# Performance work log

Hardware: AMD Instinct MI355X
Metric: run time of the kernel (lower is better)

The kernel has to match this reference:

```python
import jax, jax.numpy as jnp
import numpy as np

D_EMB = 1024
N_HEAD = 16


def setup_inputs() -> dict:
    key = jax.random.key(0)
    k0, k1, k2, k3, k4, k5 = jax.random.split(key, 6)
    B, T, D = 2, 2048, D_EMB
    s = 1.0 / np.sqrt(D)
    x = jax.random.normal(k0, (B, T, D), dtype=jnp.float32)
    # torch Linear params: weight [out, in], bias [out]
    w_attn = jax.random.normal(k1, (3 * D, D), dtype=jnp.float32) * s
    b_attn = jax.random.normal(k2, (3 * D,), dtype=jnp.float32) * 0.01
    w_proj = jax.random.normal(k3, (D, D), dtype=jnp.float32) * s
    b_proj = jax.random.normal(k4, (D,), dtype=jnp.float32) * 0.01
    return {"x": x, "w_attn": w_attn, "b_attn": b_attn,
            "w_proj": w_proj, "b_proj": b_proj}


def reference(x, w_attn, b_attn, w_proj, b_proj):
    B, T, D = x.shape
    H = N_HEAD
    hd = D // H
    qkv = x @ w_attn.T + b_attn  # [B, T, 3D]
    q, k, v = jnp.split(qkv, 3, axis=-1)
    # 'b t (h d) -> b h t d'
    q = q.reshape(B, T, H, hd).transpose(0, 2, 1, 3)
    k = k.reshape(B, T, H, hd).transpose(0, 2, 1, 3)
    v = v.reshape(B, T, H, hd).transpose(0, 2, 1, 3)
    scale = 1.0 / np.sqrt(hd)
    scores = jnp.einsum('bhid,bhjd->bhij', q, k) * scale  # [B,H,T,T]
    scores = scores.astype(jnp.float32)
    # NOTE: source applies NO causal mask despite the class name
    attn = jax.nn.softmax(scores, axis=-1)
    out = jnp.einsum('bhij,bhjd->bhid', attn, v)  # [B,H,T,hd]
    out = out.transpose(0, 2, 1, 3).reshape(B, T, D)  # 'b h i d -> b i (h d)'
    y = out @ w_proj.T + b_proj
    return y
```

## Files before the change

### kernel.cpp

```cpp
#include <hip/hip_runtime.h>


typedef unsigned short u16;
typedef __bf16  bf16x8 __attribute__((ext_vector_type(8)));
typedef float   f32x4  __attribute__((ext_vector_type(4)));
typedef float   f32x16 __attribute__((ext_vector_type(16)));
typedef unsigned short u16x8 __attribute__((ext_vector_type(8)));
typedef unsigned int   u32x4 __attribute__((ext_vector_type(4)));

__device__ __forceinline__ u16 f2bf(float f) {
  __bf16 h = (__bf16)f;
  return __builtin_bit_cast(unsigned short, h);
}
__device__ __forceinline__ float bf2f(u16 u) {
  unsigned int x = ((unsigned int)u) << 16;
  return __builtin_bit_cast(float, x);
}
__device__ __forceinline__ f32x4 mfma16(u16x8 a, u16x8 b, f32x4 c) {
  return __builtin_amdgcn_mfma_f32_16x16x32_bf16(
      __builtin_bit_cast(bf16x8, a), __builtin_bit_cast(bf16x8, b), c, 0, 0, 0);
}
__device__ __forceinline__ f32x16 mfma32(u16x8 a, u16x8 b, f32x16 c) {
  return __builtin_amdgcn_mfma_f32_32x32x16_bf16(
      __builtin_bit_cast(bf16x8, a), __builtin_bit_cast(bf16x8, b), c, 0, 0, 0);
}
__device__ __forceinline__ void gld_lds16(const void* g, void* l) {
  __builtin_amdgcn_global_load_lds(
      (const __attribute__((address_space(1))) void*)g,
      (__attribute__((address_space(3))) void*)l, 16, 0, 0);
}
__device__ __forceinline__ unsigned pack_bf2(float lo, float hi) {
  unsigned r;
  asm("v_cvt_pk_bf16_f32 %0, %1, %2" : "=v"(r) : "v"(lo), "v"(hi));
  return r;
}
__device__ __forceinline__ void xhalf(unsigned &Wl, unsigned &Wh, bool hib) {
  unsigned sel = hib ? Wl : Wh;
  unsigned p   = (unsigned)__shfl_xor((int)sel, 32);
  unsigned nl  = hib ? p  : Wl;
  unsigned nh  = hib ? Wh : p;
  Wl = nl; Wh = nh;
}

__global__ __launch_bounds__(256) void cvt_f32_bf16(
    const float* __restrict__ in, u16* __restrict__ out, int n4) {
  int i = blockIdx.x * blockDim.x + threadIdx.x;
  if (i < n4) {
    float4 v = ((const float4*)in)[i];
    ushort4 o;
    o.x = f2bf(v.x); o.y = f2bf(v.y); o.z = f2bf(v.z); o.w = f2bf(v.w);
    ((ushort4*)out)[i] = o;
  }
}

__device__ __forceinline__ void gemm_tile(
    const u16* __restrict__ A, const u16* __restrict__ B, const int K,
    const int bm, const int bn, u16* As, u16* Bs, f32x4 acc[4][4]) {
  const int tid  = threadIdx.x;
  const int lane = tid & 63;
  const int wv   = tid >> 6;
  const int wr   = wv >> 1, wc = wv & 1;
  const int g    = lane >> 4, lc = lane & 15;
  const int nk   = K >> 5;
  for (int kt = 0; kt < nk; ++kt) {
    __syncthreads();
#pragma unroll
    for (int it = 0; it < 2; ++it) {
      const int c  = it * 4 + wv;
      const int r  = c * 16 + (lane >> 2);
      const int cc = lane & 3;
      gld_lds16(A + (size_t)(bm + r) * K + kt * 32 + cc * 8, As + c * 512);
      gld_lds16(B + (size_t)(bn + r) * K + kt * 32 + cc * 8, Bs + c * 512);
    }
    __syncthreads();
    u16x8 af[4], bfv[4];
#pragma unroll
    for (int mt = 0; mt < 4; ++mt)
      af[mt] = *(const u16x8*)(As + (wr * 64 + mt * 16 + lc) * 32 + g * 8);
#pragma unroll
    for (int nt = 0; nt < 4; ++nt)
      bfv[nt] = *(const u16x8*)(Bs + (wc * 64 + nt * 16 + lc) * 32 + g * 8);
#pragma unroll
    for (int mt = 0; mt < 4; ++mt)
#pragma unroll
      for (int nt = 0; nt < 4; ++nt)
        acc[mt][nt] = mfma16(af[mt], bfv[nt], acc[mt][nt]);
  }
}

__global__ __launch_bounds__(256) void qkv_gemm(
    const u16* __restrict__ xb, const u16* __restrict__ wab,
    const float* __restrict__ b_attn,
    u16* __restrict__ Qb, u16* __restrict__ Kg, u16* __restrict__ Vg) {
  __shared__ u16 As[128 * 32], Bs[128 * 32];
  f32x4 acc[4][4];
#pragma unroll
  for (int i = 0; i < 4; ++i)
#pragma unroll
    for (int j = 0; j < 4; ++j) acc[i][j] = f32x4{0.f, 0.f, 0.f, 0.f};

  const int bn0 = blockIdx.x * 128, bm0 = blockIdx.y * 128;
  gemm_tile(xb, wab, 1024, bm0, bn0, As, Bs, acc);

  const int tid = threadIdx.x, lane = tid & 63, wv = tid >> 6;
  const int wr = wv >> 1, wc = wv & 1, g = lane >> 4, lc = lane & 15;
#pragma unroll
  for (int nt = 0; nt < 4; ++nt) {
    const int n    = bn0 + wc * 64 + nt * 16 + lc;
    const float bi = b_attn[n];
    const int sec  = n >> 10;
    const int rem  = n & 1023;
    const int h    = rem >> 6, d = rem & 63;
#pragma unroll
    for (int mt = 0; mt < 4; ++mt) {
      const int m0  = bm0 + wr * 64 + mt * 16 + g * 4;
      const int b   = m0 >> 11;
      const int t0  = m0 & 2047;
      const int bhh = b * 16 + h;
      u16 v[4];
#pragma unroll
      for (int r = 0; r < 4; ++r) v[r] = f2bf(acc[mt][nt][r] + bi);
      if (sec == 0) {
#pragma unroll
        for (int r = 0; r < 4; ++r)
          Qb[((size_t)bhh * 2048 + t0 + r) * 64 + d] = v[r];
      } else if (sec == 1) {
        const size_t kb = ((size_t)bhh * 32 + (t0 >> 6)) * 4096 +
                          (size_t)((d >> 3) * 64 + (t0 & 63)) * 8 + (d & 7);
#pragma unroll
        for (int r = 0; r < 4; ++r) Kg[kb + (size_t)r * 8] = v[r];
      } else {
        const size_t vb = ((size_t)bhh * 32 + (t0 >> 6)) * 4096 +
                          (size_t)((((t0 & 63) >> 3) * 64) + d) * 8 + (t0 & 7);
        ushort4 pk; pk.x = v[0]; pk.y = v[1]; pk.z = v[2]; pk.w = v[3];
        *(ushort4*)(Vg + vb) = pk;
      }
    }
  }
}

__global__ __launch_bounds__(256) void attn_kernel(
    const u16* __restrict__ Qb, const u16* __restrict__ Kg,
    const u16* __restrict__ Vg, u16* __restrict__ Ob) {
  __shared__ u16 Ks[2][4096];
  __shared__ u16 Vs[2][4096];

  const int tid = threadIdx.x, lane = tid & 63, wv = tid >> 6;
  const int hi = lane >> 5, l5 = lane & 31;
  const bool hib = (hi != 0);
  const int bh = blockIdx.y;
  const int qrow = blockIdx.x * 128 + wv * 32 + l5;

  const u16* Qp = Qb + ((size_t)bh * 2048 + qrow) * 64;
  const u16* Kt = Kg + (size_t)bh * 131072;
  const u16* Vt = Vg + (size_t)bh * 131072;

  const float qscale = 0.125f * 1.44269504088896f;
  u16x8 qf[4];
#pragma unroll
  for (int ks = 0; ks < 4; ++ks) {
    u16x8 raw = *(const u16x8*)(Qp + ks * 16 + hi * 8);
    u16x8 sc;
#pragma unroll
    for (int j = 0; j < 8; ++j) sc[j] = f2bf(bf2f(raw[j]) * qscale);
    qf[ks] = sc;
  }

  f32x16 o0, o1;
#pragma unroll
  for (int i = 0; i < 16; ++i) { o0[i] = 0.f; o1[i] = 0.f; }
  float m_run = -3.0e38f, l_run = 0.f;

#pragma unroll
  for (int pass = 0; pass < 2; ++pass) {
    const int cb = (pass * 4 + wv) * 64;
    gld_lds16(Kt + (size_t)(cb + lane) * 8, &Ks[0][cb * 8]);
    gld_lds16(Vt + (size_t)(cb + lane) * 8, &Vs[0][cb * 8]);
  }
  __syncthreads();

  for (int it = 0; it < 32; ++it) {
    const int cur = it & 1;
    if (it < 31) {
      const u16* Kn = Kt + (size_t)(it + 1) * 4096;
      const u16* Vn = Vt + (size_t)(it + 1) * 4096;
#pragma unroll
      for (int pass = 0; pass < 2; ++pass) {
        const int cb = (pass * 4 + wv) * 64;
        gld_lds16(Kn + (size_t)(cb + lane) * 8, &Ks[cur ^ 1][cb * 8]);
        gld_lds16(Vn + (size_t)(cb + lane) * 8, &Vs[cur ^ 1][cb * 8]);
      }
    }

    f32x16 s0, s1;
#pragma unroll
    for (int i = 0; i < 16; ++i) { s0[i] = 0.f; s1[i] = 0.f; }
    __builtin_amdgcn_s_setprio(1);
#pragma unroll
    for (int ks = 0; ks < 4; ++ks) {
      const int c = (ks * 2 + hi) * 64;
      const u16x8 kf0 = *(const u16x8*)(&Ks[cur][(c + l5) * 8]);
      const u16x8 kf1 = *(const u16x8*)(&Ks[cur][(c + 32 + l5) * 8]);
      s0 = mfma32(kf0, qf[ks], s0);
      s1 = mfma32(kf1, qf[ks], s1);
    }
    __builtin_amdgcn_s_setprio(0);

    float mx = s0[0];
#pragma unroll
    for (int i = 1; i < 16; ++i) mx = fmaxf(mx, s0[i]);
#pragma unroll
    for (int i = 0; i < 16; ++i) mx = fmaxf(mx, s1[i]);
    mx = fmaxf(mx, __shfl_xor(mx, 32));
    if (!__all(mx - m_run <= 8.0f)) {
      const float mn  = fmaxf(m_run, mx);
      const float scl = __builtin_amdgcn_exp2f(m_run - mn);
      m_run = mn;
      l_run *= scl;
#pragma unroll
      for (int i = 0; i < 16; ++i) { o0[i] *= scl; o1[i] *= scl; }
    }
    float rs = 0.f;
#pragma unroll
    for (int i = 0; i < 16; ++i) {
      s0[i] = __builtin_amdgcn_exp2f(s0[i] - m_run); rs += s0[i];
    }
#pragma unroll
    for (int i = 0; i < 16; ++i) {
      s1[i] = __builtin_amdgcn_exp2f(s1[i] - m_run); rs += s1[i];
    }
    rs += __shfl_xor(rs, 32);
    l_run += rs;

    __builtin_amdgcn_s_setprio(1);
#pragma unroll
    for (int kvt = 0; kvt < 2; ++kvt) {
      const f32x16 sp = kvt ? s1 : s0;
      unsigned W0 = pack_bf2(sp[0],  sp[1]);
      unsigned W1 = pack_bf2(sp[2],  sp[3]);
      unsigned W2 = pack_bf2(sp[4],  sp[5]);
      unsigned W3 = pack_bf2(sp[6],  sp[7]);
      unsigned W4 = pack_bf2(sp[8],  sp[9]);
      unsigned W5 = pack_bf2(sp[10], sp[11]);
      unsigned W6 = pack_bf2(sp[12], sp[13]);
      unsigned W7 = pack_bf2(sp[14], sp[15]);
      xhalf(W0, W2, hib);
      xhalf(W1, W3, hib);
      xhalf(W4, W6, hib);
      xhalf(W5, W7, hib);
      u32x4 t0; t0[0] = W0; t0[1] = W1; t0[2] = W2; t0[3] = W3;
      u32x4 t1; t1[0] = W4; t1[1] = W5; t1[2] = W6; t1[3] = W7;
      const u16x8 pf0 = __builtin_bit_cast(u16x8, t0);
      const u16x8 pf1 = __builtin_bit_cast(u16x8, t1);
      {
        const u16x8 vf0 = *(const u16x8*)(&Vs[cur][((kvt * 4 + hi) * 64 + l5) * 8]);
        const u16x8 vf1 = *(const u16x8*)(&Vs[cur][((kvt * 4 + 2 + hi) * 64 + l5) * 8]);
        o0 = mfma32(vf0, pf0, o0);
        o0 = mfma32(vf1, pf1, o0);
      }
      {
        const u16x8 vf0 = *(const u16x8*)(&Vs[cur][((kvt * 4 + hi) * 64 + 32 + l5) * 8]);
        const u16x8 vf1 = *(const u16x8*)(&Vs[cur][((kvt * 4 + 2 + hi) * 64 + 32 + l5) * 8]);
        o1 = mfma32(vf0, pf0, o1);
        o1 = mfma32(vf1, pf1, o1);
      }
    }
    __builtin_amdgcn_s_setprio(0);
    __syncthreads();
  }

  const float inv = 1.0f / l_run;
  const int b = bh >> 4, h = bh & 15;
  u16* Op = Ob + ((size_t)b * 2048 + qrow) * 1024 + h * 64;
#pragma unroll
  for (int rq = 0; rq < 4; ++rq) {
    ushort4 pk;
    pk.x = f2bf(o0[rq * 4 + 0] * inv);
    pk.y = f2bf(o0[rq * 4 + 1] * inv);
    pk.z = f2bf(o0[rq * 4 + 2] * inv);
    pk.w = f2bf(o0[rq * 4 + 3] * inv);
    *(ushort4*)(Op + rq * 8 + hi * 4) = pk;
  }
#pragma unroll
  for (int rq = 0; rq < 4; ++rq) {
    ushort4 pk;
    pk.x = f2bf(o1[rq * 4 + 0] * inv);
    pk.y = f2bf(o1[rq * 4 + 1] * inv);
    pk.z = f2bf(o1[rq * 4 + 2] * inv);
    pk.w = f2bf(o1[rq * 4 + 3] * inv);
    *(ushort4*)(Op + 32 + rq * 8 + hi * 4) = pk;
  }
}

__global__ __launch_bounds__(256) void proj_gemm(
    const u16* __restrict__ Ob, const u16* __restrict__ wpb,
    const float* __restrict__ b_proj, float* __restrict__ y) {
  __shared__ u16 As[128 * 32], Bs[128 * 32];
  f32x4 acc[4][4];
#pragma unroll
  for (int i = 0; i < 4; ++i)
#pragma unroll
    for (int j = 0; j < 4; ++j) acc[i][j] = f32x4{0.f, 0.f, 0.f, 0.f};

  const int bn0 = blockIdx.x * 128, bm0 = blockIdx.y * 128;
  gemm_tile(Ob, wpb, 1024, bm0, bn0, As, Bs, acc);

  const int tid = threadIdx.x, lane = tid & 63, wv = tid >> 6;
  const int wr = wv >> 1, wc = wv & 1, g = lane >> 4, lc = lane & 15;
#pragma unroll
  for (int nt = 0; nt < 4; ++nt) {
    const int n    = bn0 + wc * 64 + nt * 16 + lc;
    const float bi = b_proj[n];
#pragma unroll
    for (int mt = 0; mt < 4; ++mt) {
      const int m0 = bm0 + wr * 64 + mt * 16 + g * 4;
#pragma unroll
      for (int r = 0; r < 4; ++r)
        y[(size_t)(m0 + r) * 1024 + n] = acc[mt][nt][r] + bi;
    }
  }
}

extern "C" void kernel_launch(void* const* d_in, const int* in_sizes, int n_in,
                              void* d_out, int out_size, void* d_ws, size_t ws_size,
                              hipStream_t stream) {
  (void)in_sizes; (void)n_in; (void)out_size; (void)ws_size;
  const float* x      = (const float*)d_in[0];
  const float* w_attn = (const float*)d_in[1];
  const float* b_attn = (const float*)d_in[2];
  const float* w_proj = (const float*)d_in[3];
  const float* b_proj = (const float*)d_in[4];
  float* y = (float*)d_out;

  char* ws = (char*)d_ws;
  const size_t MB = 1024 * 1024;
  u16* xb  = (u16*)(ws);
  u16* wab = (u16*)(ws + 8  * MB);
  u16* wpb = (u16*)(ws + 14 * MB);
  u16* Qb  = (u16*)(ws + 16 * MB);
  u16* Kg  = (u16*)(ws + 24 * MB);
  u16* Vg  = (u16*)(ws + 32 * MB);
  u16* Ob  = (u16*)(ws + 40 * MB);

  cvt_f32_bf16<<<(4096 * 1024 / 4) / 256, 256, 0, stream>>>(x,      xb,  4096 * 1024 / 4);
  cvt_f32_bf16<<<(3072 * 1024 / 4) / 256, 256, 0, stream>>>(w_attn, wab, 3072 * 1024 / 4);
  cvt_f32_bf16<<<(1024 * 1024 / 4) / 256, 256, 0, stream>>>(w_proj, wpb, 1024 * 1024 / 4);

  qkv_gemm<<<dim3(24, 32), 256, 0, stream>>>(xb, wab, b_attn, Qb, Kg, Vg);
  attn_kernel<<<dim3(16, 32), 256, 0, stream>>>(Qb, Kg, Vg, Ob);
  proj_gemm<<<dim3(8, 32), 256, 0, stream>>>(Ob, wpb, b_proj, y);
}
```

Measured before the change: 130.9 us.

## Split KV sequence across wave pairs in attention and merge partial softmax

```diff
diff --git a/kernel.cpp b/kernel.cpp
--- a/kernel.cpp
+++ b/kernel.cpp
@@ -148,13 +148,20 @@
   const int tid = threadIdx.x, lane = tid & 63, wv = tid >> 6;
   const int hi = lane >> 5, l5 = lane & 31;
   const bool hib = (hi != 0);
+  const int qsub = wv & 1, kvh = wv >> 1;
   const int bh = blockIdx.y;
-  const int qrow = blockIdx.x * 128 + wv * 32 + l5;
+  const int qrow = blockIdx.x * 64 + qsub * 32 + l5;
 
   const u16* Qp = Qb + ((size_t)bh * 2048 + qrow) * 64;
   const u16* Kt = Kg + (size_t)bh * 131072;
   const u16* Vt = Vg + (size_t)bh * 131072;
 
+  const u16* sgb = (kvh == 0) ? Kt : Vt;
+  const u16* sg_base = (wv < 2) ? Kt : Vt;
+  u16* sl_base = (wv < 2) ? &Ks[wv & 1][0] : &Vs[wv & 1][0];
+  const int stile_off = (wv & 1) * 16;
+  (void)sgb;
+
   const float qscale = 0.125f * 1.44269504088896f;
   u16x8 qf[4];
 #pragma unroll
@@ -171,26 +178,18 @@
   for (int i = 0; i < 16; ++i) { o0[i] = 0.f; o1[i] = 0.f; }
   float m_run = -3.0e38f, l_run = 0.f;
 
-#pragma unroll
-  for (int pass = 0; pass < 2; ++pass) {
-    const int cb = (pass * 4 + wv) * 64;
-    gld_lds16(Kt + (size_t)(cb + lane) * 8, &Ks[0][cb * 8]);
-    gld_lds16(Vt + (size_t)(cb + lane) * 8, &Vs[0][cb * 8]);
-  }
-  __syncthreads();
-
-  for (int it = 0; it < 32; ++it) {
-    const int cur = it & 1;
-    if (it < 31) {
-      const u16* Kn = Kt + (size_t)(it + 1) * 4096;
-      const u16* Vn = Vt + (size_t)(it + 1) * 4096;
-#pragma unroll
-      for (int pass = 0; pass < 2; ++pass) {
-        const int cb = (pass * 4 + wv) * 64;
-        gld_lds16(Kn + (size_t)(cb + lane) * 8, &Ks[cur ^ 1][cb * 8]);
-        gld_lds16(Vn + (size_t)(cb + lane) * 8, &Vs[cur ^ 1][cb * 8]);
-      }
-    }
+  const u16* Kc = &Ks[kvh][0];
+  const u16* Vc = &Vs[kvh][0];
+
+  for (int it = 0; it < 16; ++it) {
+    __syncthreads();
+    {
+      const u16* src = sg_base + (size_t)(stile_off + it) * 4096;
+#pragma unroll
+      for (int p = 0; p < 8; ++p)
+        gld_lds16(src + p * 512 + lane * 8, sl_base + p * 512);
+    }
+    __syncthreads();
 
     f32x16 s0, s1;
 #pragma unroll
@@ -199,8 +198,8 @@
 #pragma unroll
     for (int ks = 0; ks < 4; ++ks) {
       const int c = (ks * 2 + hi) * 64;
-      const u16x8 kf0 = *(const u16x8*)(&Ks[cur][(c + l5) * 8]);
-      const u16x8 kf1 = *(const u16x8*)(&Ks[cur][(c + 32 + l5) * 8]);
+      const u16x8 kf0 = *(const u16x8*)(Kc + (c + l5) * 8);
+      const u16x8 kf1 = *(const u16x8*)(Kc + (c + 32 + l5) * 8);
       s0 = mfma32(kf0, qf[ks], s0);
       s1 = mfma32(kf1, qf[ks], s1);
     }
@@ -253,42 +252,59 @@
       const u16x8 pf0 = __builtin_bit_cast(u16x8, t0);
       const u16x8 pf1 = __builtin_bit_cast(u16x8, t1);
       {
-        const u16x8 vf0 = *(const u16x8*)(&Vs[cur][((kvt * 4 + hi) * 64 + l5) * 8]);
-        const u16x8 vf1 = *(const u16x8*)(&Vs[cur][((kvt * 4 + 2 + hi) * 64 + l5) * 8]);
+        const u16x8 vf0 = *(const u16x8*)(Vc + ((kvt * 4 + hi) * 64 + l5) * 8);
+        const u16x8 vf1 = *(const u16x8*)(Vc + ((kvt * 4 + 2 + hi) * 64 + l5) * 8);
         o0 = mfma32(vf0, pf0, o0);
         o0 = mfma32(vf1, pf1, o0);
       }
       {
-        const u16x8 vf0 = *(const u16x8*)(&Vs[cur][((kvt * 4 + hi) * 64 + 32 + l5) * 8]);
-        const u16x8 vf1 = *(const u16x8*)(&Vs[cur][((kvt * 4 + 2 + hi) * 64 + 32 + l5) * 8]);
+        const u16x8 vf0 = *(const u16x8*)(Vc + ((kvt * 4 + hi) * 64 + 32 + l5) * 8);
+        const u16x8 vf1 = *(const u16x8*)(Vc + ((kvt * 4 + 2 + hi) * 64 + 32 + l5) * 8);
         o1 = mfma32(vf0, pf0, o1);
         o1 = mfma32(vf1, pf1, o1);
       }
     }
     __builtin_amdgcn_s_setprio(0);
-    __syncthreads();
-  }
-
-  const float inv = 1.0f / l_run;
-  const int b = bh >> 4, h = bh & 15;
-  u16* Op = Ob + ((size_t)b * 2048 + qrow) * 1024 + h * 64;
-#pragma unroll
-  for (int rq = 0; rq < 4; ++rq) {
-    ushort4 pk;
-    pk.x = f2bf(o0[rq * 4 + 0] * inv);
-    pk.y = f2bf(o0[rq * 4 + 1] * inv);
-    pk.z = f2bf(o0[rq * 4 + 2] * inv);
-    pk.w = f2bf(o0[rq * 4 + 3] * inv);
-    *(ushort4*)(Op + rq * 8 + hi * 4) = pk;
-  }
-#pragma unroll
-  for (int rq = 0; rq < 4; ++rq) {
-    ushort4 pk;
-    pk.x = f2bf(o1[rq * 4 + 0] * inv);
-    pk.y = f2bf(o1[rq * 4 + 1] * inv);
-    pk.z = f2bf(o1[rq * 4 + 2] * inv);
-    pk.w = f2bf(o1[rq * 4 + 3] * inv);
-    *(ushort4*)(Op + 32 + rq * 8 + hi * 4) = pk;
+  }
+
+  __syncthreads();
+  if (kvh == 1) {
+    float* M = (qsub == 0) ? (float*)&Ks[0][0] : (float*)&Vs[0][0];
+    float* p = M + lane * 34;
+#pragma unroll
+    for (int i = 0; i < 16; ++i) { p[i] = o0[i]; p[16 + i] = o1[i]; }
+    p[32] = m_run; p[33] = l_run;
+  }
+  __syncthreads();
+  if (kvh == 0) {
+    const float* M = (qsub == 0) ? (const float*)&Ks[0][0] : (const float*)&Vs[0][0];
+    const float* p = M + lane * 34;
+    const float m2 = p[32], l2 = p[33];
+    const float mn = fmaxf(m_run, m2);
+    const float a  = __builtin_amdgcn_exp2f(m_run - mn);
+    const float b2 = __builtin_amdgcn_exp2f(m2 - mn);
+    const float l  = l_run * a + l2 * b2;
+    const float inv = 1.0f / l;
+    const int b = bh >> 4, h = bh & 15;
+    u16* Op = Ob + ((size_t)b * 2048 + qrow) * 1024 + h * 64;
+#pragma unroll
+    for (int rq = 0; rq < 4; ++rq) {
+      ushort4 pk;
+      pk.x = f2bf((o0[rq * 4 + 0] * a + p[rq * 4 + 0] * b2) * inv);
+      pk.y = f2bf((o0[rq * 4 + 1] * a + p[rq * 4 + 1] * b2) * inv);
+      pk.z = f2bf((o0[rq * 4 + 2] * a + p[rq * 4 + 2] * b2) * inv);
+      pk.w = f2bf((o0[rq * 4 + 3] * a + p[rq * 4 + 3] * b2) * inv);
+      *(ushort4*)(Op + rq * 8 + hi * 4) = pk;
+    }
+#pragma unroll
+    for (int rq = 0; rq < 4; ++rq) {
+      ushort4 pk;
+      pk.x = f2bf((o1[rq * 4 + 0] * a + p[16 + rq * 4 + 0] * b2) * inv);
+      pk.y = f2bf((o1[rq * 4 + 1] * a + p[16 + rq * 4 + 1] * b2) * inv);
+      pk.z = f2bf((o1[rq * 4 + 2] * a + p[16 + rq * 4 + 2] * b2) * inv);
+      pk.w = f2bf((o1[rq * 4 + 3] * a + p[16 + rq * 4 + 3] * b2) * inv);
+      *(ushort4*)(Op + 32 + rq * 8 + hi * 4) = pk;
+    }
   }
 }
 
@@ -347,6 +363,6 @@
   cvt_f32_bf16<<<(1024 * 1024 / 4) / 256, 256, 0, stream>>>(w_proj, wpb, 1024 * 1024 / 4);
 
   qkv_gemm<<<dim3(24, 32), 256, 0, stream>>>(xb, wab, b_attn, Qb, Kg, Vg);
-  attn_kernel<<<dim3(16, 32), 256, 0, stream>>>(Qb, Kg, Vg, Ob);
+  attn_kernel<<<dim3(32, 32), 256, 0, stream>>>(Qb, Kg, Vg, Ob);
   proj_gemm<<<dim3(8, 32), 256, 0, stream>>>(Ob, wpb, b_proj, y);
 }
```

After: 136.7 us, median of 3. 1.04x slower.

## Split attention KV range across two blocks and merge partial softmax outputs

Applied to the files above, without the earlier changes.

```diff
diff --git a/kernel.cpp b/kernel.cpp
--- a/kernel.cpp
+++ b/kernel.cpp
@@ -141,7 +141,8 @@
 
 __global__ __launch_bounds__(256) void attn_kernel(
     const u16* __restrict__ Qb, const u16* __restrict__ Kg,
-    const u16* __restrict__ Vg, u16* __restrict__ Ob) {
+    const u16* __restrict__ Vg, u16* __restrict__ P0,
+    u16* __restrict__ P1, float* __restrict__ ml) {
   __shared__ u16 Ks[2][4096];
   __shared__ u16 Vs[2][4096];
 
@@ -149,11 +150,12 @@
   const int hi = lane >> 5, l5 = lane & 31;
   const bool hib = (hi != 0);
   const int bh = blockIdx.y;
+  const int half = blockIdx.z;
   const int qrow = blockIdx.x * 128 + wv * 32 + l5;
 
   const u16* Qp = Qb + ((size_t)bh * 2048 + qrow) * 64;
-  const u16* Kt = Kg + (size_t)bh * 131072;
-  const u16* Vt = Vg + (size_t)bh * 131072;
+  const u16* Kt = Kg + (size_t)bh * 131072 + (size_t)half * 65536;
+  const u16* Vt = Vg + (size_t)bh * 131072 + (size_t)half * 65536;
 
   const float qscale = 0.125f * 1.44269504088896f;
   u16x8 qf[4];
@@ -179,9 +181,9 @@
   }
   __syncthreads();
 
-  for (int it = 0; it < 32; ++it) {
+  for (int it = 0; it < 16; ++it) {
     const int cur = it & 1;
-    if (it < 31) {
+    if (it < 15) {
       const u16* Kn = Kt + (size_t)(it + 1) * 4096;
       const u16* Vn = Vt + (size_t)(it + 1) * 4096;
 #pragma unroll
@@ -270,8 +272,7 @@
   }
 
   const float inv = 1.0f / l_run;
-  const int b = bh >> 4, h = bh & 15;
-  u16* Op = Ob + ((size_t)b * 2048 + qrow) * 1024 + h * 64;
+  u16* Pp = (half == 0 ? P0 : P1) + ((size_t)bh * 2048 + qrow) * 64;
 #pragma unroll
   for (int rq = 0; rq < 4; ++rq) {
     ushort4 pk;
@@ -279,7 +280,7 @@
     pk.y = f2bf(o0[rq * 4 + 1] * inv);
     pk.z = f2bf(o0[rq * 4 + 2] * inv);
     pk.w = f2bf(o0[rq * 4 + 3] * inv);
-    *(ushort4*)(Op + rq * 8 + hi * 4) = pk;
+    *(ushort4*)(Pp + rq * 8 + hi * 4) = pk;
   }
 #pragma unroll
   for (int rq = 0; rq < 4; ++rq) {
@@ -288,8 +289,36 @@
     pk.y = f2bf(o1[rq * 4 + 1] * inv);
     pk.z = f2bf(o1[rq * 4 + 2] * inv);
     pk.w = f2bf(o1[rq * 4 + 3] * inv);
-    *(ushort4*)(Op + 32 + rq * 8 + hi * 4) = pk;
-  }
+    *(ushort4*)(Pp + 32 + rq * 8 + hi * 4) = pk;
+  }
+  if (hi == 0) {
+    const size_t r = (size_t)half * 65536 + (size_t)bh * 2048 + qrow;
+    ml[r * 2]     = m_run;
+    ml[r * 2 + 1] = l_run;
+  }
+}
+
+__global__ __launch_bounds__(256) void attn_merge(
+    const u16* __restrict__ P0, const u16* __restrict__ P1,
+    const float* __restrict__ ml, u16* __restrict__ Ob) {
+  const int i = blockIdx.x * 256 + threadIdx.x;
+  const int row = i >> 4, c = i & 15;
+  const float m0 = ml[(size_t)row * 2],              l0 = ml[(size_t)row * 2 + 1];
+  const float m1 = ml[131072 + (size_t)row * 2],     l1 = ml[131072 + (size_t)row * 2 + 1];
+  const float mm = fmaxf(m0, m1);
+  const float w0 = l0 * __builtin_amdgcn_exp2f(m0 - mm);
+  const float w1 = l1 * __builtin_amdgcn_exp2f(m1 - mm);
+  const float inv = 1.0f / (w0 + w1);
+  const float a  = w0 * inv, b2 = w1 * inv;
+  const ushort4 p0 = *(const ushort4*)(P0 + (size_t)row * 64 + c * 4);
+  const ushort4 p1 = *(const ushort4*)(P1 + (size_t)row * 64 + c * 4);
+  ushort4 o;
+  o.x = f2bf(bf2f(p0.x) * a + bf2f(p1.x) * b2);
+  o.y = f2bf(bf2f(p0.y) * a + bf2f(p1.y) * b2);
+  o.z = f2bf(bf2f(p0.z) * a + bf2f(p1.z) * b2);
+  o.w = f2bf(bf2f(p0.w) * a + bf2f(p1.w) * b2);
+  const int b = row >> 15, h = (row >> 11) & 15, t = row & 2047;
+  *(ushort4*)(Ob + ((size_t)(b * 2048 + t)) * 1024 + h * 64 + c * 4) = o;
 }
 
 __global__ __launch_bounds__(256) void proj_gemm(
@@ -334,19 +363,23 @@
 
   char* ws = (char*)d_ws;
   const size_t MB = 1024 * 1024;
-  u16* xb  = (u16*)(ws);
-  u16* wab = (u16*)(ws + 8  * MB);
-  u16* wpb = (u16*)(ws + 14 * MB);
-  u16* Qb  = (u16*)(ws + 16 * MB);
-  u16* Kg  = (u16*)(ws + 24 * MB);
-  u16* Vg  = (u16*)(ws + 32 * MB);
-  u16* Ob  = (u16*)(ws + 40 * MB);
-
+  u16*   wpb = (u16*)(ws);
+  u16*   xb  = (u16*)(ws + 2  * MB);
+  u16*   wab = (u16*)(ws + 10 * MB);
+  float* ml  = (float*)(ws + 10 * MB);
+  u16*   Qb  = (u16*)(ws + 16 * MB);
+  u16*   Kg  = (u16*)(ws + 24 * MB);
+  u16*   Vg  = (u16*)(ws + 32 * MB);
+  u16*   P1  = (u16*)(ws + 40 * MB);
+  u16*   P0  = xb;
+  u16*   Ob  = Qb;
+
+  cvt_f32_bf16<<<(1024 * 1024 / 4) / 256, 256, 0, stream>>>(w_proj, wpb, 1024 * 1024 / 4);
   cvt_f32_bf16<<<(4096 * 1024 / 4) / 256, 256, 0, stream>>>(x,      xb,  4096 * 1024 / 4);
   cvt_f32_bf16<<<(3072 * 1024 / 4) / 256, 256, 0, stream>>>(w_attn, wab, 3072 * 1024 / 4);
-  cvt_f32_bf16<<<(1024 * 1024 / 4) / 256, 256, 0, stream>>>(w_proj, wpb, 1024 * 1024 / 4);
 
   qkv_gemm<<<dim3(24, 32), 256, 0, stream>>>(xb, wab, b_attn, Qb, Kg, Vg);
-  attn_kernel<<<dim3(16, 32), 256, 0, stream>>>(Qb, Kg, Vg, Ob);
+  attn_kernel<<<dim3(16, 32, 2), 256, 0, stream>>>(Qb, Kg, Vg, P0, P1, ml);
+  attn_merge<<<4096, 256, 0, stream>>>(P0, P1, ml, Ob);
   proj_gemm<<<dim3(8, 32), 256, 0, stream>>>(Ob, wpb, b_proj, y);
 }
```

After: 139.8 us. 6.8% more time.

## Process two KV tiles per attention iteration and remap blocks across heads

Applied to the files above, without the earlier changes.

```diff
diff --git a/kernel.cpp b/kernel.cpp
--- a/kernel.cpp
+++ b/kernel.cpp
@@ -142,14 +142,16 @@
 __global__ __launch_bounds__(256) void attn_kernel(
     const u16* __restrict__ Qb, const u16* __restrict__ Kg,
     const u16* __restrict__ Vg, u16* __restrict__ Ob) {
-  __shared__ u16 Ks[2][4096];
-  __shared__ u16 Vs[2][4096];
+  __shared__ u16 Ks[2][2][4096];
+  __shared__ u16 Vs[2][2][4096];
 
   const int tid = threadIdx.x, lane = tid & 63, wv = tid >> 6;
   const int hi = lane >> 5, l5 = lane & 31;
   const bool hib = (hi != 0);
-  const int bh = blockIdx.y;
-  const int qrow = blockIdx.x * 128 + wv * 32 + l5;
+  const int bid = blockIdx.x;
+  const int bh = (bid & 7) * 4 + ((bid >> 3) & 3);
+  const int qt = bid >> 5;
+  const int qrow = qt * 128 + wv * 32 + l5;
 
   const u16* Qp = Qb + ((size_t)bh * 2048 + qrow) * 64;
   const u16* Kt = Kg + (size_t)bh * 131072;
@@ -172,45 +174,63 @@
   float m_run = -3.0e38f, l_run = 0.f;
 
 #pragma unroll
-  for (int pass = 0; pass < 2; ++pass) {
-    const int cb = (pass * 4 + wv) * 64;
-    gld_lds16(Kt + (size_t)(cb + lane) * 8, &Ks[0][cb * 8]);
-    gld_lds16(Vt + (size_t)(cb + lane) * 8, &Vs[0][cb * 8]);
-  }
+  for (int sub = 0; sub < 2; ++sub)
+#pragma unroll
+    for (int pass = 0; pass < 2; ++pass) {
+      const int cb = (pass * 4 + wv) * 64;
+      gld_lds16(Kt + (size_t)sub * 4096 + (size_t)(cb + lane) * 8, &Ks[0][sub][cb * 8]);
+      gld_lds16(Vt + (size_t)sub * 4096 + (size_t)(cb + lane) * 8, &Vs[0][sub][cb * 8]);
+    }
   __syncthreads();
 
-  for (int it = 0; it < 32; ++it) {
+  for (int it = 0; it < 16; ++it) {
     const int cur = it & 1;
-    if (it < 31) {
-      const u16* Kn = Kt + (size_t)(it + 1) * 4096;
-      const u16* Vn = Vt + (size_t)(it + 1) * 4096;
-#pragma unroll
-      for (int pass = 0; pass < 2; ++pass) {
-        const int cb = (pass * 4 + wv) * 64;
-        gld_lds16(Kn + (size_t)(cb + lane) * 8, &Ks[cur ^ 1][cb * 8]);
-        gld_lds16(Vn + (size_t)(cb + lane) * 8, &Vs[cur ^ 1][cb * 8]);
+    if (it < 15) {
+#pragma unroll
+      for (int sub = 0; sub < 2; ++sub) {
+        const u16* Kn = Kt + (size_t)((it + 1) * 2 + sub) * 4096;
+        const u16* Vn = Vt + (size_t)((it + 1) * 2 + sub) * 4096;
+#pragma unroll
+        for (int pass = 0; pass < 2; ++pass) {
+          const int cb = (pass * 4 + wv) * 64;
+          gld_lds16(Kn + (size_t)(cb + lane) * 8, &Ks[cur ^ 1][sub][cb * 8]);
+          gld_lds16(Vn + (size_t)(cb + lane) * 8, &Vs[cur ^ 1][sub][cb * 8]);
+        }
       }
     }
 
-    f32x16 s0, s1;
-#pragma unroll
-    for (int i = 0; i < 16; ++i) { s0[i] = 0.f; s1[i] = 0.f; }
+    f32x16 s[4];
+#pragma unroll
+    for (int u = 0; u < 4; ++u)
+#pragma unroll
+      for (int i = 0; i < 16; ++i) s[u][i] = 0.f;
     __builtin_amdgcn_s_setprio(1);
 #pragma unroll
     for (int ks = 0; ks < 4; ++ks) {
       const int c = (ks * 2 + hi) * 64;
-      const u16x8 kf0 = *(const u16x8*)(&Ks[cur][(c + l5) * 8]);
-      const u16x8 kf1 = *(const u16x8*)(&Ks[cur][(c + 32 + l5) * 8]);
-      s0 = mfma32(kf0, qf[ks], s0);
-      s1 = mfma32(kf1, qf[ks], s1);
+#pragma unroll
+      for (int sub = 0; sub < 2; ++sub) {
+        const u16x8 kf0 = *(const u16x8*)(&Ks[cur][sub][(c + l5) * 8]);
+        const u16x8 kf1 = *(const u16x8*)(&Ks[cur][sub][(c + 32 + l5) * 8]);
+        s[sub * 2 + 0] = mfma32(kf0, qf[ks], s[sub * 2 + 0]);
+        s[sub * 2 + 1] = mfma32(kf1, qf[ks], s[sub * 2 + 1]);
+      }
     }
     __builtin_amdgcn_s_setprio(0);
 
-    float mx = s0[0];
-#pragma unroll
-    for (int i = 1; i < 16; ++i) mx = fmaxf(mx, s0[i]);
-#pragma unroll
-    for (int i = 0; i < 16; ++i) mx = fmaxf(mx, s1[i]);
+    float mx;
+    {
+      f32x16 t;
+#pragma unroll
+      for (int i = 0; i < 16; ++i)
+        t[i] = fmaxf(fmaxf(s[0][i], s[1][i]), fmaxf(s[2][i], s[3][i]));
+      float r8[8], r4[4];
+#pragma unroll
+      for (int i = 0; i < 8; ++i) r8[i] = fmaxf(t[i], t[i + 8]);
+#pragma unroll
+      for (int i = 0; i < 4; ++i) r4[i] = fmaxf(r8[i], r8[i + 4]);
+      mx = fmaxf(fmaxf(r4[0], r4[2]), fmaxf(r4[1], r4[3]));
+    }
     mx = fmaxf(mx, __shfl_xor(mx, 32));
     if (!__all(mx - m_run <= 8.0f)) {
       const float mn  = fmaxf(m_run, mx);
@@ -220,51 +240,62 @@
 #pragma unroll
       for (int i = 0; i < 16; ++i) { o0[i] *= scl; o1[i] *= scl; }
     }
-    float rs = 0.f;
-#pragma unroll
-    for (int i = 0; i < 16; ++i) {
-      s0[i] = __builtin_amdgcn_exp2f(s0[i] - m_run); rs += s0[i];
-    }
-#pragma unroll
-    for (int i = 0; i < 16; ++i) {
-      s1[i] = __builtin_amdgcn_exp2f(s1[i] - m_run); rs += s1[i];
+#pragma unroll
+    for (int u = 0; u < 4; ++u)
+#pragma unroll
+      for (int i = 0; i < 16; ++i)
+        s[u][i] = __builtin_amdgcn_exp2f(s[u][i] - m_run);
+    float rs;
+    {
+      f32x16 t;
+#pragma unroll
+      for (int i = 0; i < 16; ++i)
+        t[i] = (s[0][i] + s[1][i]) + (s[2][i] + s[3][i]);
+      float r8[8], r4[4];
+#pragma unroll
+      for (int i = 0; i < 8; ++i) r8[i] = t[i] + t[i + 8];
+#pragma unroll
+      for (int i = 0; i < 4; ++i) r4[i] = r8[i] + r8[i + 4];
+      rs = (r4[0] + r4[2]) + (r4[1] + r4[3]);
     }
     rs += __shfl_xor(rs, 32);
     l_run += rs;
 
     __builtin_amdgcn_s_setprio(1);
 #pragma unroll
-    for (int kvt = 0; kvt < 2; ++kvt) {
-      const f32x16 sp = kvt ? s1 : s0;
-      unsigned W0 = pack_bf2(sp[0],  sp[1]);
-      unsigned W1 = pack_bf2(sp[2],  sp[3]);
-      unsigned W2 = pack_bf2(sp[4],  sp[5]);
-      unsigned W3 = pack_bf2(sp[6],  sp[7]);
-      unsigned W4 = pack_bf2(sp[8],  sp[9]);
-      unsigned W5 = pack_bf2(sp[10], sp[11]);
-      unsigned W6 = pack_bf2(sp[12], sp[13]);
-      unsigned W7 = pack_bf2(sp[14], sp[15]);
-      xhalf(W0, W2, hib);
-      xhalf(W1, W3, hib);
-      xhalf(W4, W6, hib);
-      xhalf(W5, W7, hib);
-      u32x4 t0; t0[0] = W0; t0[1] = W1; t0[2] = W2; t0[3] = W3;
-      u32x4 t1; t1[0] = W4; t1[1] = W5; t1[2] = W6; t1[3] = W7;
-      const u16x8 pf0 = __builtin_bit_cast(u16x8, t0);
-      const u16x8 pf1 = __builtin_bit_cast(u16x8, t1);
-      {
-        const u16x8 vf0 = *(const u16x8*)(&Vs[cur][((kvt * 4 + hi) * 64 + l5) * 8]);
-        const u16x8 vf1 = *(const u16x8*)(&Vs[cur][((kvt * 4 + 2 + hi) * 64 + l5) * 8]);
-        o0 = mfma32(vf0, pf0, o0);
-        o0 = mfma32(vf1, pf1, o0);
+    for (int sub = 0; sub < 2; ++sub)
+#pragma unroll
+      for (int kvt = 0; kvt < 2; ++kvt) {
+        const f32x16 sp = s[sub * 2 + kvt];
+        unsigned W0 = pack_bf2(sp[0],  sp[1]);
+        unsigned W1 = pack_bf2(sp[2],  sp[3]);
+        unsigned W2 = pack_bf2(sp[4],  sp[5]);
+        unsigned W3 = pack_bf2(sp[6],  sp[7]);
+        unsigned W4 = pack_bf2(sp[8],  sp[9]);
+        unsigned W5 = pack_bf2(sp[10], sp[11]);
+        unsigned W6 = pack_bf2(sp[12], sp[13]);
+        unsigned W7 = pack_bf2(sp[14], sp[15]);
+        xhalf(W0, W2, hib);
+        xhalf(W1, W3, hib);
+        xhalf(W4, W6, hib);
+        xhalf(W5, W7, hib);
+        u32x4 t0; t0[0] = W0; t0[1] = W1; t0[2] = W2; t0[3] = W3;
+        u32x4 t1; t1[0] = W4; t1[1] = W5; t1[2] = W6; t1[3] = W7;
+        const u16x8 pf0 = __builtin_bit_cast(u16x8, t0);
+        const u16x8 pf1 = __builtin_bit_cast(u16x8, t1);
+        {
+          const u16x8 vf0 = *(const u16x8*)(&Vs[cur][sub][((kvt * 4 + hi) * 64 + l5) * 8]);
+          const u16x8 vf1 = *(const u16x8*)(&Vs[cur][sub][((kvt * 4 + 2 + hi) * 64 + l5) * 8]);
+          o0 = mfma32(vf0, pf0, o0);
+          o0 = mfma32(vf1, pf1, o0);
+        }
+        {
+          const u16x8 vf0 = *(const u16x8*)(&Vs[cur][sub][((kvt * 4 + hi) * 64 + 32 + l5) * 8]);
+          const u16x8 vf1 = *(const u16x8*)(&Vs[cur][sub][((kvt * 4 + 2 + hi) * 64 + 32 + l5) * 8]);
+          o1 = mfma32(vf0, pf0, o1);
+          o1 = mfma32(vf1, pf1, o1);
+        }
       }
-      {
-        const u16x8 vf0 = *(const u16x8*)(&Vs[cur][((kvt * 4 + hi) * 64 + 32 + l5) * 8]);
-        const u16x8 vf1 = *(const u16x8*)(&Vs[cur][((kvt * 4 + 2 + hi) * 64 + 32 + l5) * 8]);
-        o1 = mfma32(vf0, pf0, o1);
-        o1 = mfma32(vf1, pf1, o1);
-      }
-    }
     __builtin_amdgcn_s_setprio(0);
     __syncthreads();
   }
@@ -347,6 +378,6 @@
   cvt_f32_bf16<<<(1024 * 1024 / 4) / 256, 256, 0, stream>>>(w_proj, wpb, 1024 * 1024 / 4);
 
   qkv_gemm<<<dim3(24, 32), 256, 0, stream>>>(xb, wab, b_attn, Qb, Kg, Vg);
-  attn_kernel<<<dim3(16, 32), 256, 0, stream>>>(Qb, Kg, Vg, Ob);
+  attn_kernel<<<512, 256, 0, stream>>>(Qb, Kg, Vg, Ob);
   proj_gemm<<<dim3(8, 32), 256, 0, stream>>>(Ob, wpb, b_proj, y);
 }
```

Result: no change. 128.4 us (-1.9%).
